# Performance work log

Hardware: AMD Instinct MI355X
Metric: run time of the kernel (lower is better)

The kernel has to match this reference:

```python
import jax, jax.numpy as jnp
import numpy as np

D_MODEL = 1024
NUM_HEADS = 16
HEAD_DIM = D_MODEL // NUM_HEADS
THETA = 10000.0
BATCH, SEQ = 2, 2048


def rope(x, token_positions):
    # x: [b, h, s, d]; token_positions: [s]
    d = x.shape[-1]
    freqs = 1.0 / THETA ** (jnp.arange(0, d, 2, dtype=jnp.float32)[: d // 2] / d)
    ang = token_positions.astype(jnp.float32)[:, None] * freqs[None, :]  # [s, d/2]
    cos, sin = jnp.cos(ang), jnp.sin(ang)
    xr = x.reshape(*x.shape[:-1], d // 2, 2)
    x_even, x_odd = xr[..., 0], xr[..., 1]
    out_even = x_even * cos - x_odd * sin
    out_odd = x_even * sin + x_odd * cos
    return jnp.stack([out_even, out_odd], axis=-1).reshape(x.shape)


def setup_inputs() -> dict:
    key = jax.random.key(0)
    ks = jax.random.split(key, 5)
    std = np.sqrt(2.0 / (D_MODEL + D_MODEL))
    mk = lambda k: (jax.random.truncated_normal(k, -3.0, 3.0, (D_MODEL, D_MODEL), jnp.float32) * std)
    return {
        "x": jax.random.normal(ks[0], (BATCH, SEQ, D_MODEL), jnp.float32),
        "Wq": mk(ks[1]),
        "Wk": mk(ks[2]),
        "Wv": mk(ks[3]),
        "Wo": mk(ks[4]),
        "casual_mask": jnp.tril(jnp.ones((SEQ, SEQ), dtype=bool)),
        "token_positions": jnp.arange(SEQ, dtype=jnp.int32),
    }


def reference(x, Wq, Wk, Wv, Wo, casual_mask, token_positions):
    b, s, _ = x.shape
    split = lambda t: t.reshape(b, s, NUM_HEADS, HEAD_DIM).transpose(0, 2, 1, 3)
    q = split(x @ Wq.T)  # [b, h, s, d]
    k = split(x @ Wk.T)
    v = split(x @ Wv.T)
    q = rope(q, token_positions)
    k = rope(k, token_positions)
    scores = jnp.einsum("bhqd,bhkd->bhqk", q, k) / np.sqrt(HEAD_DIM)
    scores = jnp.where(casual_mask, scores, -jnp.inf)
    probs = jax.nn.softmax(scores, axis=-1)
    out = jnp.einsum("bhqk,bhkd->bhqd", probs, v)
    out = out.transpose(0, 2, 1, 3).reshape(b, s, D_MODEL)
    return out @ Wo.T
```

## Files before the change

### kernel.cpp

```cpp
#include <hip/hip_runtime.h>
#include <hip/hip_bf16.h>

#define SEQ_LEN 2048
#define NBATCH 2
#define DM 1024
#define NH 16
#define HD 64
#define NR (NBATCH * SEQ_LEN)
#define NQKV (3 * DM)
#define LDQK 2048

typedef __attribute__((ext_vector_type(8))) short bf16x8;
typedef __attribute__((ext_vector_type(4))) float f32x4;
typedef __attribute__((ext_vector_type(16))) float f32x16;

__device__ __forceinline__ short f2b(float f) {
    __hip_bfloat16 h = __float2bfloat16(f);
    return *reinterpret_cast<short*>(&h);
}

__device__ __forceinline__ void gload_lds16(const void* g, void* l) {
    __builtin_amdgcn_global_load_lds(
        (const __attribute__((address_space(1))) unsigned int*)g,
        (__attribute__((address_space(3))) unsigned int*)l, 16, 0, 0);
}

__global__ __launch_bounds__(256) void cvt_all(
    const float* __restrict__ x,  const float* __restrict__ wq,
    const float* __restrict__ wk, const float* __restrict__ wv,
    const float* __restrict__ wo,
    __hip_bfloat16* __restrict__ xb, __hip_bfloat16* __restrict__ wqkvb,
    __hip_bfloat16* __restrict__ wob) {
    int id = blockIdx.x;
    const float* src; __hip_bfloat16* dst;
    if (id < 4096) { src = x + (size_t)id * 1024; dst = xb + (size_t)id * 1024; }
    else {
        int k = id - 4096, seg = k >> 10;
        size_t off = (size_t)(k & 1023) * 1024;
        if      (seg == 0) { src = wq + off; dst = wqkvb + off; }
        else if (seg == 1) { src = wk + off; dst = wqkvb + (1u << 20) + off; }
        else if (seg == 2) { src = wv + off; dst = wqkvb + (2u << 20) + off; }
        else               { src = wo + off; dst = wob + off; }
    }
    int i = threadIdx.x * 4;
    float4 v = *(const float4*)(src + i);
    dst[i + 0] = __float2bfloat16(v.x);
    dst[i + 1] = __float2bfloat16(v.y);
    dst[i + 2] = __float2bfloat16(v.z);
    dst[i + 3] = __float2bfloat16(v.w);
}

__global__ __launch_bounds__(512) void gemm256_qkv(
    const __hip_bfloat16* __restrict__ A,
    const __hip_bfloat16* __restrict__ B,
    __hip_bfloat16* __restrict__ C,
    __hip_bfloat16* __restrict__ Vtg,
    const int* __restrict__ pos) {
    __shared__ __hip_bfloat16 As[2][2][64 * 128];
    __shared__ __hip_bfloat16 Bs[2][2][64 * 128];

    const int t    = threadIdx.x;
    const int wave = t >> 6;
    const int wm   = wave >> 2;
    const int wn   = wave & 3;
    const int lane = t & 63;
    const int quad = lane >> 4;
    const int l16  = lane & 15;
    const int K    = DM;
    const int NT   = K >> 6;
    const int NI   = K >> 7;

    const int wg = (blockIdx.x & 7) * 24 + (blockIdx.x >> 3);
    const int bx = wg & 15;
    const int by = wg >> 4;
    const int m0 = bx * 256, n0 = by * 256;

    const int  t16  = t * 16;
    const int  scx8 = ((t & 7) ^ ((t >> 3) & 7)) * 8;
    const int  srA  = t >> 3;
    const int  gB   = (t >> 8) & 1;
    const int  rB   = (t >> 3) & 31;

#define STAGE_A(BUF, HM, TT)                                                    \
    {                                                                           \
        const __hip_bfloat16* _s =                                              \
            A + (size_t)(m0 + (HM) * 64 + srA) * K + (TT) * 64 + scx8;          \
        gload_lds16(_s,               (char*)As[BUF][HM] + t16);                \
        gload_lds16(_s + (size_t)128 * K, (char*)As[BUF][HM] + t16 + 8192);     \
    }
#define STAGE_B(BUF, HN, TT)                                                    \
    {                                                                           \
        const __hip_bfloat16* _s =                                              \
            B + (size_t)(n0 + gB * 64 + (HN) * 32 + rB) * K + (TT) * 64 + scx8; \
        gload_lds16(_s,               (char*)Bs[BUF][HN] + t16);                \
        gload_lds16(_s + (size_t)128 * K, (char*)Bs[BUF][HN] + t16 + 8192);     \
    }
#define LDA(BUF, HM, AF)                                                        \
    _Pragma("unroll") for (int rb = 0; rb < 4; rb++)                            \
    _Pragma("unroll") for (int kk = 0; kk < 2; kk++)                            \
        AF[rb][kk] = *(const bf16x8*)((const char*)As[BUF][HM] +                \
            (wm * 64 + rb * 16 + l16) * 128 + (((kk * 4 + quad) ^ (l16 & 7)) << 4));
#define LDB(BUF, HN, BF)                                                        \
    _Pragma("unroll") for (int cb = 0; cb < 2; cb++)                            \
    _Pragma("unroll") for (int kk = 0; kk < 2; kk++)                            \
        BF[cb][kk] = *(const bf16x8*)((const char*)Bs[BUF][HN] +                \
            (wn * 32 + cb * 16 + l16) * 128 + (((kk * 4 + quad) ^ (l16 & 7)) << 4));
#define MM(HM, HN, AF, BF)                                                      \
    {                                                                           \
        __builtin_amdgcn_s_setprio(1);                                          \
        _Pragma("unroll") for (int rb = 0; rb < 4; rb++)                        \
        _Pragma("unroll") for (int cb = 0; cb < 2; cb++) {                      \
            acc[HM][HN][rb][cb] = __builtin_amdgcn_mfma_f32_16x16x32_bf16(      \
                AF[rb][0], BF[cb][0], acc[HM][HN][rb][cb], 0, 0, 0);            \
            acc[HM][HN][rb][cb] = __builtin_amdgcn_mfma_f32_16x16x32_bf16(      \
                AF[rb][1], BF[cb][1], acc[HM][HN][rb][cb], 0, 0, 0);            \
        }                                                                       \
        __builtin_amdgcn_s_setprio(0);                                          \
    }
#define VM0 asm volatile("s_waitcnt vmcnt(0)" ::: "memory")
#define VM4 asm volatile("s_waitcnt vmcnt(4)" ::: "memory")
#define VM6 asm volatile("s_waitcnt vmcnt(6)" ::: "memory")
#define LGKM0 asm volatile("s_waitcnt lgkmcnt(0)" ::: "memory")
#define SCHED0 __builtin_amdgcn_sched_barrier(0)
#define BARR __builtin_amdgcn_s_barrier()
#define GATE_A SCHED0; BARR; LGKM0; SCHED0

    f32x4 acc[2][2][4][2];
#pragma unroll
    for (int a_ = 0; a_ < 2; a_++)
#pragma unroll
        for (int b_ = 0; b_ < 2; b_++)
#pragma unroll
            for (int c_ = 0; c_ < 4; c_++)
#pragma unroll
                for (int d_ = 0; d_ < 2; d_++)
                    acc[a_][b_][c_][d_] = (f32x4){0.f, 0.f, 0.f, 0.f};

    STAGE_A(0, 0, 0); STAGE_A(0, 1, 0); STAGE_B(0, 0, 0); STAGE_B(0, 1, 0);
    STAGE_A(1, 0, 1); STAGE_B(1, 0, 1); STAGE_A(1, 1, 1);
    VM6;
    BARR;

    for (int i = 0; i < NI; ++i) {
        const int TB = 2 * i + 1, T2 = 2 * i + 2, T3 = 2 * i + 3;
        const bool s2 = T2 < NT, s3 = T3 < NT;
        bf16x8 a[4][2], b0[2][2], b1[2][2];

        LDA(0, 0, a); LDB(0, 0, b0);
        STAGE_B(1, 1, TB);
        GATE_A;
        MM(0, 0, a, b0);
        BARR;
        LDB(0, 1, b1);
        if (s2) STAGE_A(0, 0, T2);
        GATE_A;
        MM(0, 1, a, b1);
        BARR;
        LDA(0, 1, a); LDB(0, 0, b0);
        GATE_A;
        MM(1, 0, a, b0);
        BARR;
        LDB(0, 1, b1);
        if (s2) STAGE_B(0, 0, T2);
        GATE_A;
        MM(1, 1, a, b1);
        if (i < NI - 1) { VM4; } else { VM0; }
        BARR;
        LDA(1, 0, a); LDB(1, 0, b0);
        if (s2) STAGE_A(0, 1, T2);
        GATE_A;
        MM(0, 0, a, b0);
        BARR;
        LDB(1, 1, b1);
        if (s2) STAGE_B(0, 1, T2);
        if (s3) STAGE_A(1, 0, T3);
        GATE_A;
        MM(0, 1, a, b1);
        BARR;
        LDA(1, 1, a); LDB(1, 0, b0);
        GATE_A;
        MM(1, 0, a, b0);
        BARR;
        LDB(1, 1, b1);
        if (s3) { STAGE_B(1, 0, T3); STAGE_A(1, 1, T3); }
        GATE_A;
        MM(1, 1, a, b1);
        if (i < NI - 1) { VM6; }
        BARR;
    }
#undef STAGE_A
#undef STAGE_B
#undef LDA
#undef LDB
#undef MM
#undef VM0
#undef VM4
#undef VM6
#undef LGKM0
#undef SCHED0
#undef BARR
#undef GATE_A

    if (by < 8) {
        const float sc = (by < 4) ? 0.125f : 1.0f;
        float fr[2][2];
#pragma unroll
        for (int hn = 0; hn < 2; hn++)
#pragma unroll
            for (int cb = 0; cb < 2; cb++)
                fr[hn][cb] = __expf(-(float)((hn * 32 + cb * 16 + l16) & ~1) *
                                    (9.210340371976184f / 64.0f));
        const float par = (l16 & 1) ? 1.f : -1.f;
#pragma unroll
        for (int hm = 0; hm < 2; hm++)
#pragma unroll
            for (int rb = 0; rb < 4; rb++)
#pragma unroll
                for (int r = 0; r < 4; r++) {
                    int row = m0 + wm * 128 + hm * 64 + rb * 16 + quad * 4 + r;
                    float p = (float)pos[row & (SEQ_LEN - 1)];
#pragma unroll
                    for (int hn = 0; hn < 2; hn++)
#pragma unroll
                        for (int cb = 0; cb < 2; cb++) {
                            float sn, cs;
                            __sincosf(p * fr[hn][cb], &sn, &cs);
                            float v  = acc[hm][hn][rb][cb][r];
                            float pt = __shfl_xor(v, 1);
                            C[(size_t)row * LDQK + n0 + wn * 64 + hn * 32 + cb * 16 + l16] =
                                __float2bfloat16((v * cs + par * pt * sn) * sc);
                        }
                }
    } else {
#pragma unroll
        for (int hm = 0; hm < 2; hm++)
#pragma unroll
            for (int rb = 0; rb < 4; rb++) {
                int row0e = m0 + wm * 128 + hm * 64 + rb * 16 + quad * 4;
                int bb = row0e >> 11, ss = row0e & (SEQ_LEN - 1);
                int ssw = (ss & ~12) | ((ss & 4) << 1) | ((ss & 8) >> 1);
#pragma unroll
                for (int hn = 0; hn < 2; hn++)
#pragma unroll
                    for (int cb = 0; cb < 2; cb++) {
                        int vcol = n0 + wn * 64 + hn * 32 + cb * 16 + l16 - 2048;
                        int hh = vcol >> 6, dd = vcol & 63;
                        ushort4 u;
                        u.x = (unsigned short)f2b(acc[hm][hn][rb][cb][0]);
                        u.y = (unsigned short)f2b(acc[hm][hn][rb][cb][1]);
                        u.z = (unsigned short)f2b(acc[hm][hn][rb][cb][2]);
                        u.w = (unsigned short)f2b(acc[hm][hn][rb][cb][3]);
                        *(ushort4*)(Vtg + ((size_t)(bb * NH + hh) * HD + dd) * SEQ_LEN + ssw) = u;
                    }
            }
    }
}

__global__ __launch_bounds__(256) void gemm_op(
    const __hip_bfloat16* __restrict__ A,
    const __hip_bfloat16* __restrict__ B,
    float* __restrict__ C) {
    __shared__ __hip_bfloat16 As[2][64 * 32];
    __shared__ __hip_bfloat16 Bs[2][128 * 32];
    const int t    = threadIdx.x;
    const int wave = t >> 6;
    const int lane = t & 63;
    const int quad = lane >> 4;
    const int l16  = lane & 15;
    const int wy = wave >> 1, wx = wave & 1;
    const int K = DM;

    const int wg = (blockIdx.x & 7) * 64 + (blockIdx.x >> 3);
    const int m0 = (wg & 63) * 64;
    const int n0 = (wg >> 6) * 128;

    const int sr  = t >> 2;
    const int scx = (t & 3) ^ (sr & 3);

    const __hip_bfloat16* Ag = A + (size_t)(m0 + sr) * K + scx * 8;
    const __hip_bfloat16* Bg = B + (size_t)(n0 + sr) * K + scx * 8;

#define OSTAGE(BUF, K0)                                                         \
    {                                                                           \
        gload_lds16(Ag + (K0), (char*)As[BUF] + t * 16);                        \
        gload_lds16(Bg + (K0), (char*)Bs[BUF] + t * 16);                        \
        gload_lds16(Bg + (size_t)64 * K + (K0), (char*)Bs[BUF] + (t + 256) * 16); \
    }

    f32x4 acc[2][4];
#pragma unroll
    for (int i = 0; i < 2; i++)
#pragma unroll
        for (int j = 0; j < 4; j++) acc[i][j] = (f32x4){0.f, 0.f, 0.f, 0.f};

    const int NT = K >> 5;
    OSTAGE(0, 0);
    __syncthreads();
    int cur = 0;
    for (int t32 = 0; t32 < NT; ++t32) {
        if (t32 + 1 < NT) OSTAGE(cur ^ 1, (t32 + 1) * 32);

        bf16x8 af[2], bfr[4];
#pragma unroll
        for (int rb = 0; rb < 2; rb++) {
            int row = wy * 32 + rb * 16 + l16;
            af[rb] = *(const bf16x8*)((const char*)As[cur] + row * 64 +
                                      ((quad ^ (row & 3)) << 4));
        }
#pragma unroll
        for (int cb = 0; cb < 4; cb++) {
            int row = wx * 64 + cb * 16 + l16;
            bfr[cb] = *(const bf16x8*)((const char*)Bs[cur] + row * 64 +
                                       ((quad ^ (row & 3)) << 4));
        }
#pragma unroll
        for (int rb = 0; rb < 2; rb++)
#pragma unroll
            for (int cb = 0; cb < 4; cb++)
                acc[rb][cb] = __builtin_amdgcn_mfma_f32_16x16x32_bf16(
                    af[rb], bfr[cb], acc[rb][cb], 0, 0, 0);

        __syncthreads();
        cur ^= 1;
    }
#undef OSTAGE

#pragma unroll
    for (int rb = 0; rb < 2; rb++)
#pragma unroll
        for (int r = 0; r < 4; r++) {
            size_t ro = (size_t)(m0 + wy * 32 + rb * 16 + quad * 4 + r) * DM;
#pragma unroll
            for (int cb = 0; cb < 4; cb++)
                C[ro + n0 + wx * 64 + cb * 16 + l16] = acc[rb][cb][r];
        }
}

__global__ __launch_bounds__(256, 2) void attn_kernel(
    const __hip_bfloat16* __restrict__ QK,
    const __hip_bfloat16* __restrict__ Vtg,
    __hip_bfloat16* __restrict__ O) {
    __shared__ __hip_bfloat16 Ks[2][64 * 64];
    __shared__ __hip_bfloat16 Vs[2][64 * 64];

    const int t    = threadIdx.x;
    const int wave = t >> 6;
    const int lane = t & 63;
    const int l5   = lane & 31;
    const int hi   = lane >> 5;
    const int id   = blockIdx.x;
    const int qtc  = id >> 5;
    const int hb   = id & 31;
    const int h    = hb & 15;
    const int b    = hb >> 4;
    const int qt   = (qtc < 8) ? (15 - 2 * qtc) : (14 - 2 * (qtc - 8));

    const int row0 = qt * 128 + wave * 32;
    const int ktd  = (row0 + 31) >> 6;
    const int KTM  = 2 * qt + 1;

    const int sr  = t >> 3;
    const int scx = (t & 7) ^ (sr & 7);

    const __hip_bfloat16* kbase = QK + (size_t)(b * SEQ_LEN) * LDQK + DM + h * HD;
    const __hip_bfloat16* vbase = Vtg + (size_t)((b * NH + h) * HD) * SEQ_LEN;

    bf16x8 qf[4];
    {
        const __hip_bfloat16* qp =
            QK + (size_t)(b * SEQ_LEN + row0 + l5) * LDQK + h * HD + hi * 8;
#pragma unroll
        for (int dc = 0; dc < 4; dc++) qf[dc] = *(const bf16x8*)(qp + dc * 16);
    }

    f32x16 o0a, o0b, o1a, o1b;
#pragma unroll
    for (int i = 0; i < 16; i++) { o0a[i] = 0.f; o0b[i] = 0.f; o1a[i] = 0.f; o1b[i] = 0.f; }
    float l_acc = 0.f;

#define STAGE(BUF, KT)                                                          \
    {                                                                           \
        gload_lds16(kbase + (size_t)((KT) * 64 + sr) * LDQK + scx * 8,          \
                    (char*)&Ks[BUF][0] + t * 16);                               \
        gload_lds16(kbase + (size_t)((KT) * 64 + sr + 32) * LDQK + scx * 8,     \
                    (char*)&Ks[BUF][0] + (t + 256) * 16);                       \
        gload_lds16(vbase + (size_t)sr * SEQ_LEN + (KT) * 64 + scx * 8,         \
                    (char*)&Vs[BUF][0] + t * 16);                               \
        gload_lds16(vbase + (size_t)(sr + 32) * SEQ_LEN + (KT) * 64 + scx * 8,  \
                    (char*)&Vs[BUF][0] + (t + 256) * 16);                       \
    }

#define LFRAG(BASE, ROW, CH)                                                    \
    (*(const bf16x8*)((const char*)(BASE) + (ROW) * 128 + ((((CH) ^ ((ROW) & 7))) << 4)))

#define MKPA(S, PA0, PA1)                                                       \
    {                                                                           \
        float p_[16];                                                           \
        _Pragma("unroll") for (int r = 0; r < 16; r++) {                        \
            p_[r] = __expf((S)[r]);                                             \
            l_acc += p_[r];                                                     \
        }                                                                       \
        _Pragma("unroll") for (int j = 0; j < 8; j++) {                         \
            PA0[j] = f2b(p_[j]);                                                \
            PA1[j] = f2b(p_[8 + j]);                                            \
        }                                                                       \
    }

#define TRIP(BUF, KT)                                                           \
    {                                                                           \
        f32x16 s0, s1;                                                          \
        _Pragma("unroll") for (int i = 0; i < 16; i++) { s0[i] = 0.f; s1[i] = 0.f; } \
        __builtin_amdgcn_s_setprio(1);                                          \
        _Pragma("unroll") for (int dc = 0; dc < 4; dc++) {                      \
            bf16x8 k0f = LFRAG(Ks[BUF], l5, dc * 2 + hi);                       \
            bf16x8 k1f = LFRAG(Ks[BUF], 32 + l5, dc * 2 + hi);                  \
            s0 = __builtin_amdgcn_mfma_f32_32x32x16_bf16(k0f, qf[dc], s0, 0, 0, 0); \
            s1 = __builtin_amdgcn_mfma_f32_32x32x16_bf16(k1f, qf[dc], s1, 0, 0, 0); \
        }                                                                       \
        __builtin_amdgcn_s_setprio(0);                                          \
        if ((KT) == ktd) {                                                      \
            int qrow = row0 + l5;                                               \
            _Pragma("unroll") for (int r = 0; r < 16; r++) {                    \
                int key = (KT) * 64 + (r & 3) + 8 * (r >> 2) + 4 * hi;          \
                if (key > qrow) s0[r] = -1e30f;                                 \
                if (key + 32 > qrow) s1[r] = -1e30f;                            \
            }                                                                   \
        }                                                                       \
        bf16x8 pa0, pa1, pa2, pa3;                                              \
        MKPA(s0, pa0, pa1);                                                     \
        MKPA(s1, pa2, pa3);                                                     \
        __builtin_amdgcn_s_setprio(1);                                          \
        _Pragma("unroll") for (int kc = 0; kc < 2; kc++) {                      \
            bf16x8 v0f = LFRAG(Vs[BUF], l5, kc * 2 + hi);                       \
            bf16x8 v1f = LFRAG(Vs[BUF], 32 + l5, kc * 2 + hi);                  \
            bf16x8 paf = (kc == 0) ? pa0 : pa1;                                 \
            o0a = __builtin_amdgcn_mfma_f32_32x32x16_bf16(paf, v0f, o0a, 0, 0, 0); \
            o1a = __builtin_amdgcn_mfma_f32_32x32x16_bf16(paf, v1f, o1a, 0, 0, 0); \
        }                                                                       \
        _Pragma("unroll") for (int kc = 2; kc < 4; kc++) {                      \
            bf16x8 v0f = LFRAG(Vs[BUF], l5, kc * 2 + hi);                       \
            bf16x8 v1f = LFRAG(Vs[BUF], 32 + l5, kc * 2 + hi);                  \
            bf16x8 paf = (kc == 2) ? pa2 : pa3;                                 \
            o0b = __builtin_amdgcn_mfma_f32_32x32x16_bf16(paf, v0f, o0b, 0, 0, 0); \
            o1b = __builtin_amdgcn_mfma_f32_32x32x16_bf16(paf, v1f, o1b, 0, 0, 0); \
        }                                                                       \
        __builtin_amdgcn_s_setprio(0);                                          \
    }

    STAGE(0, 0);
    for (int kt = 0; kt <= KTM; ++kt) {
        const int buf = kt & 1;
        __syncthreads();
        if (kt < KTM) STAGE(buf ^ 1, kt + 1);
        if (kt <= ktd) TRIP(buf, kt);
    }

    l_acc += __shfl_xor(l_acc, 32);
    float inv = 1.0f / l_acc;
#pragma unroll
    for (int r = 0; r < 16; r++) {
        int crow  = (r & 3) + 8 * (r >> 2) + 4 * hi;
        float invr = __shfl(inv, crow);
        size_t ro = (size_t)(b * SEQ_LEN + row0 + crow) * DM + h * HD;
        O[ro + l5]      = __float2bfloat16((o0a[r] + o0b[r]) * invr);
        O[ro + 32 + l5] = __float2bfloat16((o1a[r] + o1b[r]) * invr);
    }
#undef STAGE
#undef LFRAG
#undef MKPA
#undef TRIP
}

extern "C" void kernel_launch(void* const* d_in, const int* in_sizes, int n_in,
                              void* d_out, int out_size, void* d_ws, size_t ws_size,
                              hipStream_t stream) {
    const float* x  = (const float*)d_in[0];
    const float* Wq = (const float*)d_in[1];
    const float* Wk = (const float*)d_in[2];
    const float* Wv = (const float*)d_in[3];
    const float* Wo = (const float*)d_in[4];
    const int* pos = (const int*)d_in[6];
    float* out = (float*)d_out;

    char* w = (char*)d_ws;
    const size_t MiB = 1024 * 1024;
    __hip_bfloat16* xb    = (__hip_bfloat16*)(w + 0 * MiB);
    __hip_bfloat16* Ab    = (__hip_bfloat16*)(w + 0 * MiB);
    __hip_bfloat16* Wqkvb = (__hip_bfloat16*)(w + 8 * MiB);
    __hip_bfloat16* Wob   = (__hip_bfloat16*)(w + 14 * MiB);
    __hip_bfloat16* QKb   = (__hip_bfloat16*)(w + 16 * MiB);
    __hip_bfloat16* Vtg   = (__hip_bfloat16*)(w + 32 * MiB);

    cvt_all<<<8192, 256, 0, stream>>>(x, Wq, Wk, Wv, Wo, xb, Wqkvb, Wob);

    gemm256_qkv<<<192, 512, 0, stream>>>(xb, Wqkvb, QKb, Vtg, pos);

    attn_kernel<<<512, 256, 0, stream>>>(QKb, Vtg, Ab);

    gemm_op<<<512, 256, 0, stream>>>(Ab, Wob, out);
}
```

Measured before the change: 198.9 us.

## Retile QKV GEMM to 256x192 tiles for 256 workgroups

Changes the fused QKV projection GEMM tile from 256x256 to 256x192, so the grid grows from 192 to 256 workgroups and matches the CU count more closely. B staging is split into a 128-row and a 64-row LDS buffer, each wave computes 48 columns (three 16-wide blocks), and the RoPE/V-transpose epilogue now decides per 16-column block whether it is Q/K or V. This is meant to remove idle CUs from the partial wave of tiles, at the cost of lower arithmetic intensity per tile and a less uniform epilogue.

```diff
diff --git a/kernel.cpp b/kernel.cpp
--- a/kernel.cpp
+++ b/kernel.cpp
@@ -50,14 +50,15 @@
     dst[i + 3] = __float2bfloat16(v.w);
 }
 
-__global__ __launch_bounds__(512) void gemm256_qkv(
+__global__ __launch_bounds__(512) void gemm_qkv(
     const __hip_bfloat16* __restrict__ A,
     const __hip_bfloat16* __restrict__ B,
     __hip_bfloat16* __restrict__ C,
     __hip_bfloat16* __restrict__ Vtg,
     const int* __restrict__ pos) {
-    __shared__ __hip_bfloat16 As[2][2][64 * 128];
-    __shared__ __hip_bfloat16 Bs[2][2][64 * 128];
+    __shared__ __hip_bfloat16 As[2][2][128 * 64];
+    __shared__ __hip_bfloat16 Bs01[2][128 * 64];
+    __shared__ __hip_bfloat16 Bs2[2][64 * 64];
 
     const int t    = threadIdx.x;
     const int wave = t >> 6;
@@ -70,50 +71,71 @@
     const int NT   = K >> 6;
     const int NI   = K >> 7;
 
-    const int wg = (blockIdx.x & 7) * 24 + (blockIdx.x >> 3);
+    const int wg = (blockIdx.x & 7) * 32 + (blockIdx.x >> 3);
     const int bx = wg & 15;
     const int by = wg >> 4;
-    const int m0 = bx * 256, n0 = by * 256;
-
-    const int  t16  = t * 16;
-    const int  scx8 = ((t & 7) ^ ((t >> 3) & 7)) * 8;
-    const int  srA  = t >> 3;
-    const int  gB   = (t >> 8) & 1;
-    const int  rB   = (t >> 3) & 31;
+    const int m0 = bx * 256, n0 = by * 192;
+
+    const int t16  = t * 16;
+    const int scx8 = ((t & 7) ^ ((t >> 3) & 7)) * 8;
+    const int srA  = t >> 3;
+    const int gB01 = (((t >> 3) >> 5) * 48) + ((t >> 3) & 31);
+    const int gB2  = (((t >> 3) >> 4) * 48) + 32 + ((t >> 3) & 15);
 
 #define STAGE_A(BUF, HM, TT)                                                    \
     {                                                                           \
         const __hip_bfloat16* _s =                                              \
             A + (size_t)(m0 + (HM) * 64 + srA) * K + (TT) * 64 + scx8;          \
-        gload_lds16(_s,               (char*)As[BUF][HM] + t16);                \
+        gload_lds16(_s,                   (char*)As[BUF][HM] + t16);            \
         gload_lds16(_s + (size_t)128 * K, (char*)As[BUF][HM] + t16 + 8192);     \
     }
-#define STAGE_B(BUF, HN, TT)                                                    \
+#define STAGE_B01(BUF, TT)                                                      \
     {                                                                           \
         const __hip_bfloat16* _s =                                              \
-            B + (size_t)(n0 + gB * 64 + (HN) * 32 + rB) * K + (TT) * 64 + scx8; \
-        gload_lds16(_s,               (char*)Bs[BUF][HN] + t16);                \
-        gload_lds16(_s + (size_t)128 * K, (char*)Bs[BUF][HN] + t16 + 8192);     \
+            B + (size_t)(n0 + gB01) * K + (TT) * 64 + scx8;                     \
+        gload_lds16(_s,                  (char*)Bs01[BUF] + t16);               \
+        gload_lds16(_s + (size_t)96 * K, (char*)Bs01[BUF] + t16 + 8192);        \
+    }
+#define STAGE_B2(BUF, TT)                                                       \
+    {                                                                           \
+        const __hip_bfloat16* _s =                                              \
+            B + (size_t)(n0 + gB2) * K + (TT) * 64 + scx8;                      \
+        gload_lds16(_s, (char*)Bs2[BUF] + t16);                                 \
     }
 #define LDA(BUF, HM, AF)                                                        \
     _Pragma("unroll") for (int rb = 0; rb < 4; rb++)                            \
     _Pragma("unroll") for (int kk = 0; kk < 2; kk++)                            \
         AF[rb][kk] = *(const bf16x8*)((const char*)As[BUF][HM] +                \
             (wm * 64 + rb * 16 + l16) * 128 + (((kk * 4 + quad) ^ (l16 & 7)) << 4));
-#define LDB(BUF, HN, BF)                                                        \
+#define LDB01(BUF, BF)                                                          \
     _Pragma("unroll") for (int cb = 0; cb < 2; cb++)                            \
     _Pragma("unroll") for (int kk = 0; kk < 2; kk++)                            \
-        BF[cb][kk] = *(const bf16x8*)((const char*)Bs[BUF][HN] +                \
+        BF[cb][kk] = *(const bf16x8*)((const char*)Bs01[BUF] +                  \
             (wn * 32 + cb * 16 + l16) * 128 + (((kk * 4 + quad) ^ (l16 & 7)) << 4));
-#define MM(HM, HN, AF, BF)                                                      \
+#define LDB2(BUF, BF)                                                           \
+    _Pragma("unroll") for (int kk = 0; kk < 2; kk++)                            \
+        BF[kk] = *(const bf16x8*)((const char*)Bs2[BUF] +                       \
+            (wn * 16 + l16) * 128 + (((kk * 4 + quad) ^ (l16 & 7)) << 4));
+#define MM16(HM, AF, BF)                                                        \
     {                                                                           \
         __builtin_amdgcn_s_setprio(1);                                          \
         _Pragma("unroll") for (int rb = 0; rb < 4; rb++)                        \
         _Pragma("unroll") for (int cb = 0; cb < 2; cb++) {                      \
-            acc[HM][HN][rb][cb] = __builtin_amdgcn_mfma_f32_16x16x32_bf16(      \
-                AF[rb][0], BF[cb][0], acc[HM][HN][rb][cb], 0, 0, 0);            \
-            acc[HM][HN][rb][cb] = __builtin_amdgcn_mfma_f32_16x16x32_bf16(      \
-                AF[rb][1], BF[cb][1], acc[HM][HN][rb][cb], 0, 0, 0);            \
+            acc[HM][cb][rb] = __builtin_amdgcn_mfma_f32_16x16x32_bf16(          \
+                AF[rb][0], BF[cb][0], acc[HM][cb][rb], 0, 0, 0);                \
+            acc[HM][cb][rb] = __builtin_amdgcn_mfma_f32_16x16x32_bf16(          \
+                AF[rb][1], BF[cb][1], acc[HM][cb][rb], 0, 0, 0);                \
+        }                                                                       \
+        __builtin_amdgcn_s_setprio(0);                                          \
+    }
+#define MM8(HM, AF, BF)                                                         \
+    {                                                                           \
+        __builtin_amdgcn_s_setprio(1);                                          \
+        _Pragma("unroll") for (int rb = 0; rb < 4; rb++) {                      \
+            acc[HM][2][rb] = __builtin_amdgcn_mfma_f32_16x16x32_bf16(           \
+                AF[rb][0], BF[0], acc[HM][2][rb], 0, 0, 0);                     \
+            acc[HM][2][rb] = __builtin_amdgcn_mfma_f32_16x16x32_bf16(           \
+                AF[rb][1], BF[1], acc[HM][2][rb], 0, 0, 0);                     \
         }                                                                       \
         __builtin_amdgcn_s_setprio(0);                                          \
     }
@@ -125,74 +147,75 @@
 #define BARR __builtin_amdgcn_s_barrier()
 #define GATE_A SCHED0; BARR; LGKM0; SCHED0
 
-    f32x4 acc[2][2][4][2];
+    f32x4 acc[2][3][4];
 #pragma unroll
     for (int a_ = 0; a_ < 2; a_++)
 #pragma unroll
-        for (int b_ = 0; b_ < 2; b_++)
+        for (int b_ = 0; b_ < 3; b_++)
 #pragma unroll
             for (int c_ = 0; c_ < 4; c_++)
-#pragma unroll
-                for (int d_ = 0; d_ < 2; d_++)
-                    acc[a_][b_][c_][d_] = (f32x4){0.f, 0.f, 0.f, 0.f};
-
-    STAGE_A(0, 0, 0); STAGE_A(0, 1, 0); STAGE_B(0, 0, 0); STAGE_B(0, 1, 0);
-    STAGE_A(1, 0, 1); STAGE_B(1, 0, 1); STAGE_A(1, 1, 1);
+                acc[a_][b_][c_] = (f32x4){0.f, 0.f, 0.f, 0.f};
+
+    STAGE_A(0, 0, 0); STAGE_A(0, 1, 0); STAGE_B01(0, 0); STAGE_B2(0, 0);
+    STAGE_A(1, 0, 1); STAGE_B01(1, 1); STAGE_A(1, 1, 1);
     VM6;
     BARR;
 
     for (int i = 0; i < NI; ++i) {
         const int TB = 2 * i + 1, T2 = 2 * i + 2, T3 = 2 * i + 3;
         const bool s2 = T2 < NT, s3 = T3 < NT;
-        bf16x8 a[4][2], b0[2][2], b1[2][2];
-
-        LDA(0, 0, a); LDB(0, 0, b0);
-        STAGE_B(1, 1, TB);
-        GATE_A;
-        MM(0, 0, a, b0);
-        BARR;
-        LDB(0, 1, b1);
+        bf16x8 a[4][2], b01[2][2], b2[2];
+
+        LDA(0, 0, a); LDB01(0, b01);
+        STAGE_B2(1, TB);
+        GATE_A;
+        MM16(0, a, b01);
+        BARR;
+        LDB2(0, b2);
         if (s2) STAGE_A(0, 0, T2);
         GATE_A;
-        MM(0, 1, a, b1);
-        BARR;
-        LDA(0, 1, a); LDB(0, 0, b0);
-        GATE_A;
-        MM(1, 0, a, b0);
-        BARR;
-        LDB(0, 1, b1);
-        if (s2) STAGE_B(0, 0, T2);
-        GATE_A;
-        MM(1, 1, a, b1);
+        MM8(0, a, b2);
+        BARR;
+        LDA(0, 1, a); LDB01(0, b01);
+        GATE_A;
+        MM16(1, a, b01);
+        BARR;
+        LDB2(0, b2);
+        if (s2) STAGE_B01(0, T2);
+        GATE_A;
+        MM8(1, a, b2);
         if (i < NI - 1) { VM4; } else { VM0; }
         BARR;
-        LDA(1, 0, a); LDB(1, 0, b0);
+        LDA(1, 0, a); LDB01(1, b01);
         if (s2) STAGE_A(0, 1, T2);
         GATE_A;
-        MM(0, 0, a, b0);
-        BARR;
-        LDB(1, 1, b1);
-        if (s2) STAGE_B(0, 1, T2);
+        MM16(0, a, b01);
+        BARR;
+        LDB2(1, b2);
+        if (s2) STAGE_B2(0, T2);
         if (s3) STAGE_A(1, 0, T3);
         GATE_A;
-        MM(0, 1, a, b1);
-        BARR;
-        LDA(1, 1, a); LDB(1, 0, b0);
-        GATE_A;
-        MM(1, 0, a, b0);
-        BARR;
-        LDB(1, 1, b1);
-        if (s3) { STAGE_B(1, 0, T3); STAGE_A(1, 1, T3); }
-        GATE_A;
-        MM(1, 1, a, b1);
+        MM8(0, a, b2);
+        BARR;
+        LDA(1, 1, a); LDB01(1, b01);
+        GATE_A;
+        MM16(1, a, b01);
+        BARR;
+        LDB2(1, b2);
+        if (s3) { STAGE_B01(1, T3); STAGE_A(1, 1, T3); }
+        GATE_A;
+        MM8(1, a, b2);
         if (i < NI - 1) { VM6; }
         BARR;
     }
 #undef STAGE_A
-#undef STAGE_B
+#undef STAGE_B01
+#undef STAGE_B2
 #undef LDA
-#undef LDB
-#undef MM
+#undef LDB01
+#undef LDB2
+#undef MM16
+#undef MM8
 #undef VM0
 #undef VM4
 #undef VM6
@@ -201,59 +224,50 @@
 #undef BARR
 #undef GATE_A
 
-    if (by < 8) {
-        const float sc = (by < 4) ? 0.125f : 1.0f;
-        float fr[2][2];
-#pragma unroll
-        for (int hn = 0; hn < 2; hn++)
-#pragma unroll
-            for (int cb = 0; cb < 2; cb++)
-                fr[hn][cb] = __expf(-(float)((hn * 32 + cb * 16 + l16) & ~1) *
-                                    (9.210340371976184f / 64.0f));
-        const float par = (l16 & 1) ? 1.f : -1.f;
-#pragma unroll
-        for (int hm = 0; hm < 2; hm++)
-#pragma unroll
-            for (int rb = 0; rb < 4; rb++)
-#pragma unroll
-                for (int r = 0; r < 4; r++) {
-                    int row = m0 + wm * 128 + hm * 64 + rb * 16 + quad * 4 + r;
-                    float p = (float)pos[row & (SEQ_LEN - 1)];
-#pragma unroll
-                    for (int hn = 0; hn < 2; hn++)
-#pragma unroll
-                        for (int cb = 0; cb < 2; cb++) {
-                            float sn, cs;
-                            __sincosf(p * fr[hn][cb], &sn, &cs);
-                            float v  = acc[hm][hn][rb][cb][r];
-                            float pt = __shfl_xor(v, 1);
-                            C[(size_t)row * LDQK + n0 + wn * 64 + hn * 32 + cb * 16 + l16] =
-                                __float2bfloat16((v * cs + par * pt * sn) * sc);
-                        }
+    const float RC = 9.210340371976184f / 64.0f;
+    float fr[3], sc[3];
+    bool isv[3];
+#pragma unroll
+    for (int cb = 0; cb < 3; cb++) {
+        int cbase = n0 + wn * 48 + cb * 16;
+        isv[cb] = cbase >= 2048;
+        sc[cb]  = (cbase < 1024) ? 0.125f : 1.0f;
+        fr[cb]  = __expf(-(float)(((cbase + l16) & 63) & ~1) * RC);
+    }
+    const float par = (l16 & 1) ? 1.f : -1.f;
+#pragma unroll
+    for (int hm = 0; hm < 2; hm++)
+#pragma unroll
+        for (int rb = 0; rb < 4; rb++) {
+            int rbase = m0 + wm * 128 + hm * 64 + rb * 16 + quad * 4;
+            int bb = rbase >> 11, ss = rbase & (SEQ_LEN - 1);
+            int ssw = (ss & ~12) | ((ss & 4) << 1) | ((ss & 8) >> 1);
+#pragma unroll
+            for (int cb = 0; cb < 3; cb++) {
+                if (!isv[cb]) {
+#pragma unroll
+                    for (int r = 0; r < 4; r++) {
+                        int row = rbase + r;
+                        float p = (float)pos[row & (SEQ_LEN - 1)];
+                        float sn, cs;
+                        __sincosf(p * fr[cb], &sn, &cs);
+                        float v  = acc[hm][cb][rb][r];
+                        float pt = __shfl_xor(v, 1);
+                        C[(size_t)row * LDQK + n0 + wn * 48 + cb * 16 + l16] =
+                            __float2bfloat16((v * cs + par * pt * sn) * sc[cb]);
+                    }
+                } else {
+                    int vc = n0 + wn * 48 + cb * 16 + l16 - 2048;
+                    int hh = vc >> 6, dd = vc & 63;
+                    ushort4 u;
+                    u.x = (unsigned short)f2b(acc[hm][cb][rb][0]);
+                    u.y = (unsigned short)f2b(acc[hm][cb][rb][1]);
+                    u.z = (unsigned short)f2b(acc[hm][cb][rb][2]);
+                    u.w = (unsigned short)f2b(acc[hm][cb][rb][3]);
+                    *(ushort4*)(Vtg + ((size_t)(bb * NH + hh) * HD + dd) * SEQ_LEN + ssw) = u;
                 }
-    } else {
-#pragma unroll
-        for (int hm = 0; hm < 2; hm++)
-#pragma unroll
-            for (int rb = 0; rb < 4; rb++) {
-                int row0e = m0 + wm * 128 + hm * 64 + rb * 16 + quad * 4;
-                int bb = row0e >> 11, ss = row0e & (SEQ_LEN - 1);
-                int ssw = (ss & ~12) | ((ss & 4) << 1) | ((ss & 8) >> 1);
-#pragma unroll
-                for (int hn = 0; hn < 2; hn++)
-#pragma unroll
-                    for (int cb = 0; cb < 2; cb++) {
-                        int vcol = n0 + wn * 64 + hn * 32 + cb * 16 + l16 - 2048;
-                        int hh = vcol >> 6, dd = vcol & 63;
-                        ushort4 u;
-                        u.x = (unsigned short)f2b(acc[hm][hn][rb][cb][0]);
-                        u.y = (unsigned short)f2b(acc[hm][hn][rb][cb][1]);
-                        u.z = (unsigned short)f2b(acc[hm][hn][rb][cb][2]);
-                        u.w = (unsigned short)f2b(acc[hm][hn][rb][cb][3]);
-                        *(ushort4*)(Vtg + ((size_t)(bb * NH + hh) * HD + dd) * SEQ_LEN + ssw) = u;
-                    }
             }
-    }
+        }
 }
 
 __global__ __launch_bounds__(256) void gemm_op(
@@ -493,7 +507,7 @@
 
     cvt_all<<<8192, 256, 0, stream>>>(x, Wq, Wk, Wv, Wo, xb, Wqkvb, Wob);
 
-    gemm256_qkv<<<192, 512, 0, stream>>>(xb, Wqkvb, QKb, Vtg, pos);
+    gemm_qkv<<<256, 512, 0, stream>>>(xb, Wqkvb, QKb, Vtg, pos);
 
     attn_kernel<<<512, 256, 0, stream>>>(QKb, Vtg, Ab);
 
```

Measured after the change: 198.2 us. About the same (-0.4%).
